# Kernel optimization log

Hardware: AMD Instinct MI355X
Metric: run time of the kernel (lower is better)

## Reference

```python
import jax, jax.numpy as jnp
import numpy as np

N_HEAD = 16
N_EMBD = 1024
HEAD_DIM = N_EMBD // N_HEAD
ROPE_BASE = 10000.0


def _rms_norm(x):
    # F.rms_norm with eps=None uses dtype eps
    eps = jnp.finfo(x.dtype).eps
    ms = jnp.mean(jnp.square(x), axis=-1, keepdims=True)
    return x * jax.lax.rsqrt(ms + eps)


def _rope_tables(T, dtype):
    inv_freq = 1.0 / (ROPE_BASE ** (jnp.arange(0, HEAD_DIM, 2, dtype=jnp.float32) / HEAD_DIM))
    t = jnp.arange(T, dtype=jnp.float32)
    freqs = jnp.outer(t, inv_freq)  # [T, D/2]
    cos = jnp.cos(freqs).astype(dtype)[None, :, None, :]  # [1,T,1,D/2]
    sin = jnp.sin(freqs).astype(dtype)[None, :, None, :]
    return cos, sin


def _apply_rotary(x, cos, sin):
    d = x.shape[-1] // 2
    x1, x2 = x[..., :d], x[..., d:]
    y1 = x1 * cos + x2 * sin
    y2 = -x1 * sin + x2 * cos
    return jnp.concatenate([y1, y2], axis=-1).astype(x.dtype)


def setup_inputs() -> dict:
    key = jax.random.key(0)
    ks = jax.random.split(key, 7)
    B, T, C = 4, 2048, N_EMBD
    s = 0.02
    return {
        "x": jax.random.normal(ks[0], (B, T, C), dtype=jnp.float32),
        "v1": jax.random.normal(ks[1], (B, T, C), dtype=jnp.float32),
        "Wq": jax.random.normal(ks[2], (C, C), dtype=jnp.float32) * s,
        "Wk": jax.random.normal(ks[3], (C, C), dtype=jnp.float32) * s,
        "Wv": jax.random.normal(ks[4], (C, C), dtype=jnp.float32) * s,
        "Wproj": jax.random.normal(ks[5], (C, C), dtype=jnp.float32) * s,
        "lamb": jnp.float32(0.5),
    }


def reference(x, v1, Wq, Wk, Wv, Wproj, lamb):
    B, T, C = x.shape
    H, D = N_HEAD, HEAD_DIM
    q = (x @ Wq.T).reshape(B, T, H, D)
    k = (x @ Wk.T).reshape(B, T, H, D)
    v = (x @ Wv.T).reshape(B, T, H, D)
    # value-lambda residual mix
    v = (1.0 - lamb) * v + lamb * v1.reshape(B, T, H, D)
    # RMSNorm then RoPE on q, k
    cos, sin = _rope_tables(T, x.dtype)
    q = _apply_rotary(_rms_norm(q), cos, sin)
    k = _apply_rotary(_rms_norm(k), cos, sin)
    # causal SDPA
    scale = 1.0 / jnp.sqrt(jnp.float32(D)).astype(x.dtype)
    scores = jnp.einsum("bthd,bshd->bhts", q, k) * scale  # [B,H,T,T]
    causal = jnp.tril(jnp.ones((T, T), dtype=bool))
    scores = jnp.where(causal[None, None], scores, jnp.finfo(scores.dtype).min)
    attn = jax.nn.softmax(scores, axis=-1)
    y = jnp.einsum("bhts,bshd->bthd", attn, v).reshape(B, T, C)
    y = y @ Wproj.T
    return (y, v1)
```

## Files before the change

kernel.cpp:

```cpp
#include <hip/hip_runtime.h>
#include <hip/hip_bf16.h>

typedef __bf16 bf16x8 __attribute__((ext_vector_type(8)));
typedef __bf16 bf16x4 __attribute__((ext_vector_type(4)));
typedef float  f32x4  __attribute__((ext_vector_type(4)));
typedef unsigned u32x4 __attribute__((ext_vector_type(4)));

#define B_ 4
#define T_ 2048
#define H_ 16
#define D_ 64
#define C_ 1024
#define M_ 8192
#define NE_ ((size_t)M_ * C_)

__global__ void probe_dtype(const unsigned short* __restrict__ x,
                            int* __restrict__ flag)
{
  __shared__ float red[256];
  float m = 0.0f;
  for (int i = threadIdx.x; i < 4096; i += 256) {
    unsigned int u = ((unsigned int)x[i]) << 16;
    float v = fabsf(__uint_as_float(u));
    if (!(v <= 1e30f)) v = 1e31f;
    m = fmaxf(m, v);
  }
  red[threadIdx.x] = m;
  __syncthreads();
  for (int s = 128; s > 0; s >>= 1) {
    if (threadIdx.x < s) red[threadIdx.x] = fmaxf(red[threadIdx.x], red[threadIdx.x + s]);
    __syncthreads();
  }
  if (threadIdx.x == 0) *flag = (red[0] > 100.0f) ? 1 : 0;
}

__device__ __forceinline__ float load1_adapt(const void* p, size_t idx, int f)
{
  if (f) return ((const float*)p)[idx];
  return __bfloat162float(((const __hip_bfloat16*)p)[idx]);
}

__global__ __launch_bounds__(256) void cvt_bf16(
    const int* __restrict__ flagp, const void* __restrict__ src,
    __bf16* __restrict__ dst, int n)
{
  const int f = *flagp;
  for (size_t i = ((size_t)blockIdx.x * 256 + threadIdx.x) * 8; i < (size_t)n;
       i += (size_t)gridDim.x * 2048) {
    bf16x8 r;
    if (f) {
      const float* pf = (const float*)src + i;
      float4 a = *(const float4*)pf;
      float4 b = *(const float4*)(pf + 4);
      r[0] = (__bf16)a.x; r[1] = (__bf16)a.y; r[2] = (__bf16)a.z; r[3] = (__bf16)a.w;
      r[4] = (__bf16)b.x; r[5] = (__bf16)b.y; r[6] = (__bf16)b.z; r[7] = (__bf16)b.w;
    } else {
      r = *(const bf16x8*)((const __bf16*)src + i);
    }
    *(bf16x8*)(dst + i) = r;
  }
}

__device__ __forceinline__ void g2lds16(const __bf16* g, __bf16* l)
{
  __builtin_amdgcn_global_load_lds(
      (const __attribute__((address_space(1))) void*)g,
      (__attribute__((address_space(3))) void*)l, 16, 0, 0);
}

__device__ __forceinline__ unsigned cvtpk_bf16(float lo, float hi)
{
  unsigned r;
  asm("v_cvt_pk_bf16_f32 %0, %1, %2" : "=v"(r) : "v"(lo), "v"(hi));
  return r;
}

__global__ __launch_bounds__(256) void gemm128(
    const __bf16* __restrict__ A, const __bf16* __restrict__ Bm,
    void* __restrict__ C, int M, int N, int K,
    const int* __restrict__ flagp, int adaptive)
{
  __shared__ __bf16 As[128][64];
  __shared__ __bf16 Bs[128][64];

  const int tid  = threadIdx.x;
  const int wv   = tid >> 6;
  const int lane = tid & 63;
  const int n16  = lane & 15;
  const int quad = lane >> 4;
  const int wm = (wv & 1) * 64, wn = (wv >> 1) * 64;

  const int nwgx = gridDim.x;
  const int id   = blockIdx.y * nwgx + blockIdx.x;
  const int cpx  = (nwgx * gridDim.y) >> 3;
  const int swz  = (id & 7) * cpx + (id >> 3);
  const int m0 = (swz % nwgx) * 128, n0 = (swz / nwgx) * 128;

  f32x4 acc[4][4];
#pragma unroll
  for (int i = 0; i < 4; i++)
#pragma unroll
    for (int j = 0; j < 4; j++) acc[i][j] = (f32x4){0.f, 0.f, 0.f, 0.f};

  const int trow = tid >> 3;
  const int tcol = (tid & 7) * 8;

  for (int k0 = 0; k0 < K; k0 += 64) {
#pragma unroll
    for (int p = 0; p < 4; p++) {
      g2lds16(A  + (size_t)(m0 + trow + p * 32) * K + k0 + tcol,
              &As[trow + p * 32][tcol]);
      g2lds16(Bm + (size_t)(n0 + trow + p * 32) * K + k0 + tcol,
              &Bs[trow + p * 32][tcol]);
    }
    __syncthreads();

#pragma unroll
    for (int kk = 0; kk < 2; kk++) {
      bf16x8 af[4], bf[4];
#pragma unroll
      for (int i = 0; i < 4; i++) {
        af[i] = *(const bf16x8*)&As[wm + i * 16 + n16][kk * 32 + quad * 8];
        bf[i] = *(const bf16x8*)&Bs[wn + i * 16 + n16][kk * 32 + quad * 8];
      }
#pragma unroll
      for (int i = 0; i < 4; i++)
#pragma unroll
        for (int j = 0; j < 4; j++)
          acc[i][j] = __builtin_amdgcn_mfma_f32_16x16x32_bf16(af[i], bf[j],
                                                              acc[i][j], 0, 0, 0);
    }
    __syncthreads();
  }

  const int f = adaptive ? *flagp : 0;
  const int rb = quad * 4;
#pragma unroll
  for (int i = 0; i < 4; i++)
#pragma unroll
    for (int j = 0; j < 4; j++)
#pragma unroll
      for (int r = 0; r < 4; r++) {
        const size_t idx = (size_t)(m0 + wm + i * 16 + rb + r) * N
                           + n0 + wn + j * 16 + n16;
        if (f) ((float*)C)[idx] = acc[i][j][r];
        else   ((__bf16*)C)[idx] = (__bf16)acc[i][j][r];
      }
}

__global__ __launch_bounds__(256) void fuse_rope_vmix(
    const int* __restrict__ flagp,
    __hip_bfloat16* __restrict__ q,
    __hip_bfloat16* __restrict__ k,
    __hip_bfloat16* __restrict__ v,
    const void* __restrict__ v1,
    const void* __restrict__ lambp)
{
  const int f    = *flagp;
  const int task = blockIdx.x * 4 + (threadIdx.x >> 6);
  const int lane = threadIdx.x & 63;
  const int h  = task & 15;
  const int bt = task >> 4;
  const int t  = bt & (T_ - 1);
  const size_t base = (size_t)bt * C_ + h * D_ + lane;

  const int j = lane & 31;
  const float inv = expf(-(float)j * (9.2103403719761836f / 32.0f));
  const float ang = (float)t * inv;
  const float cs = cosf(ang), sn = sinf(ang);
  const float EPS = 0.0078125f;

  {
    float xv = __bfloat162float(q[base]);
    float ss = xv * xv;
#pragma unroll
    for (int off = 32; off >= 1; off >>= 1) ss += __shfl_xor(ss, off);
    float r  = rsqrtf(ss * (1.0f / 64.0f) + EPS);
    float xn = xv * r;
    float pr = __shfl_xor(xn, 32);
    float yv = (lane < 32) ? (xn * cs + pr * sn) : (pr * -sn + xn * cs);
    q[base] = __float2bfloat16(yv);
  }
  {
    float xv = __bfloat162float(k[base]);
    float ss = xv * xv;
#pragma unroll
    for (int off = 32; off >= 1; off >>= 1) ss += __shfl_xor(ss, off);
    float r  = rsqrtf(ss * (1.0f / 64.0f) + EPS);
    float xn = xv * r;
    float pr = __shfl_xor(xn, 32);
    float yv = (lane < 32) ? (xn * cs + pr * sn) : (pr * -sn + xn * cs);
    k[base] = __float2bfloat16(yv);
  }
  {
    float lam = load1_adapt(lambp, 0, f);
    float vv  = __bfloat162float(v[base]);
    float v1v = load1_adapt(v1, base, f);
    v[base] = __float2bfloat16((1.0f - lam) * vv + lam * v1v);
  }
}

__global__ __launch_bounds__(256) void attn_mfma(
    const __bf16* q,
    const __bf16* __restrict__ k,
    const __bf16* __restrict__ v,
    __bf16* y)
{
  __shared__ alignas(16) __bf16 Ks[64][72];
  __shared__ alignas(16) __bf16 VTs[64][88];

  const int tid  = threadIdx.x;
  const int wv   = tid >> 6;
  const int lane = tid & 63;
  const int n16  = lane & 15;
  const int quad = lane >> 4;
  const int b = blockIdx.y >> 4, h = blockIdx.y & 15;
  const int q0 = (gridDim.x - 1 - blockIdx.x) * 128;
  const size_t hb = (size_t)b * T_ * C_ + h * D_;

  bf16x8 aq[2][2];
#pragma unroll
  for (int rt = 0; rt < 2; rt++) {
    const size_t qoff = hb + (size_t)(q0 + wv * 32 + rt * 16 + n16) * C_;
    aq[rt][0] = *(const bf16x8*)(q + qoff + quad * 8);
    aq[rt][1] = *(const bf16x8*)(q + qoff + 32 + quad * 8);
#pragma unroll
    for (int jj = 0; jj < 8; jj++) {
      aq[rt][0][jj] = (__bf16)((float)aq[rt][0][jj] * 0.125f);
      aq[rt][1][jj] = (__bf16)((float)aq[rt][1][jj] * 0.125f);
    }
  }

  f32x4 Ot[2][4];
  float l_lane[2];
#pragma unroll
  for (int rt = 0; rt < 2; rt++) {
    l_lane[rt] = 0.0f;
#pragma unroll
    for (int t = 0; t < 4; t++) Ot[rt][t] = (f32x4){0.f, 0.f, 0.f, 0.f};
  }

  const int trow = tid >> 2;
  const int tcol = (tid & 3) * 16;

  const int srcA = n16 + 32 * (quad & 1);
  const int srcB = srcA + 16;
  const bool lowq = quad < 2;

  const int niter = q0 / 64 + 2;

  bf16x8 kr0, kr1, vr0, vr1;
  {
    const __bf16* ks = k + hb + (size_t)trow * C_ + tcol;
    kr0 = *(const bf16x8*)(ks);
    kr1 = *(const bf16x8*)(ks + 8);
    const __bf16* vs = v + hb + (size_t)lane * C_;
    vr0 = *(const bf16x8*)(vs + wv * 8);
    vr1 = *(const bf16x8*)(vs + (wv + 4) * 8);
    *(bf16x8*)&Ks[trow][tcol]     = kr0;
    *(bf16x8*)&Ks[trow][tcol + 8] = kr1;
#pragma unroll
    for (int jj = 0; jj < 8; jj++) VTs[wv * 8 + jj][lane] = vr0[jj];
#pragma unroll
    for (int jj = 0; jj < 8; jj++) VTs[(wv + 4) * 8 + jj][lane] = vr1[jj];
  }
  __syncthreads();

  for (int it = 0; it < niter; it++) {
    const int s0 = it * 64;
    const bool havenext = (it + 1 < niter);

    if (havenext) {
      const int sn = s0 + 64;
      const __bf16* ks = k + hb + (size_t)(sn + trow) * C_ + tcol;
      kr0 = *(const bf16x8*)(ks);
      kr1 = *(const bf16x8*)(ks + 8);
      const __bf16* vs = v + hb + (size_t)(sn + lane) * C_;
      vr0 = *(const bf16x8*)(vs + wv * 8);
      vr1 = *(const bf16x8*)(vs + (wv + 4) * 8);
    }

    if (s0 <= q0 + wv * 32 + 31) {
#pragma unroll
      for (int rt = 0; rt < 2; rt++) {
        const int rbase = q0 + wv * 32 + rt * 16;
        if (s0 <= rbase + 15) {
          f32x4 S[4];
          __builtin_amdgcn_s_setprio(1);
#pragma unroll
          for (int t = 0; t < 4; t++) {
            S[t] = (f32x4){0.f, 0.f, 0.f, 0.f};
            bf16x8 b0 = *(const bf16x8*)&Ks[t * 16 + n16][quad * 8];
            bf16x8 b1 = *(const bf16x8*)&Ks[t * 16 + n16][32 + quad * 8];
            S[t] = __builtin_amdgcn_mfma_f32_16x16x32_bf16(b0, aq[rt][0], S[t], 0, 0, 0);
            S[t] = __builtin_amdgcn_mfma_f32_16x16x32_bf16(b1, aq[rt][1], S[t], 0, 0, 0);
          }
          __builtin_amdgcn_s_setprio(0);

          if (s0 + 63 > rbase) {
            const int tg = rbase + n16;
#pragma unroll
            for (int t = 0; t < 4; t++) {
#pragma unroll
              for (int r = 0; r < 4; r++) {
                const int sg = s0 + t * 16 + quad * 4 + r;
                if (sg > tg) S[t][r] = -1e30f;
              }
            }
          }

          float p[4][4];
#pragma unroll
          for (int t = 0; t < 4; t++)
#pragma unroll
            for (int r = 0; r < 4; r++)
              p[t][r] = __expf(S[t][r] - 8.0f);
          l_lane[rt] += ((p[0][0] + p[0][1]) + (p[0][2] + p[0][3]))
                      + ((p[1][0] + p[1][1]) + (p[1][2] + p[1][3]))
                      + ((p[2][0] + p[2][1]) + (p[2][2] + p[2][3]))
                      + ((p[3][0] + p[3][1]) + (p[3][2] + p[3][3]));

          unsigned pk0[4], pk1[4];
#pragma unroll
          for (int t = 0; t < 4; t++) {
            pk0[t] = cvtpk_bf16(p[t][0], p[t][1]);
            pk1[t] = cvtpk_bf16(p[t][2], p[t][3]);
          }

          bf16x8 pf[2];
#pragma unroll
          for (int c = 0; c < 2; c++) {
            const int tE = 2 * c, tO = 2 * c + 1;
            unsigned a0 = (unsigned)__shfl((int)pk0[tE], srcA);
            unsigned a1 = (unsigned)__shfl((int)pk0[tO], srcA);
            unsigned b0 = (unsigned)__shfl((int)pk1[tE], srcA);
            unsigned b1 = (unsigned)__shfl((int)pk1[tO], srcA);
            unsigned c0 = (unsigned)__shfl((int)pk0[tE], srcB);
            unsigned c1 = (unsigned)__shfl((int)pk0[tO], srcB);
            unsigned d0 = (unsigned)__shfl((int)pk1[tE], srcB);
            unsigned d1 = (unsigned)__shfl((int)pk1[tO], srcB);
            union { u32x4 u; bf16x8 b; } uw;
            uw.u[0] = lowq ? a0 : a1;
            uw.u[1] = lowq ? b0 : b1;
            uw.u[2] = lowq ? c0 : c1;
            uw.u[3] = lowq ? d0 : d1;
            pf[c] = uw.b;
          }

          __builtin_amdgcn_s_setprio(1);
#pragma unroll
          for (int t = 0; t < 4; t++) {
            bf16x8 va0 = *(const bf16x8*)&VTs[t * 16 + n16][quad * 8];
            bf16x8 va1 = *(const bf16x8*)&VTs[t * 16 + n16][32 + quad * 8];
            Ot[rt][t] = __builtin_amdgcn_mfma_f32_16x16x32_bf16(va0, pf[0], Ot[rt][t], 0, 0, 0);
            Ot[rt][t] = __builtin_amdgcn_mfma_f32_16x16x32_bf16(va1, pf[1], Ot[rt][t], 0, 0, 0);
          }
          __builtin_amdgcn_s_setprio(0);
        }
      }
    }

    __syncthreads();
    if (havenext) {
      *(bf16x8*)&Ks[trow][tcol]     = kr0;
      *(bf16x8*)&Ks[trow][tcol + 8] = kr1;
#pragma unroll
      for (int jj = 0; jj < 8; jj++) VTs[wv * 8 + jj][lane] = vr0[jj];
#pragma unroll
      for (int jj = 0; jj < 8; jj++) VTs[(wv + 4) * 8 + jj][lane] = vr1[jj];
    }
    __syncthreads();
  }

#pragma unroll
  for (int rt = 0; rt < 2; rt++) {
    float lt = l_lane[rt];
    lt += __shfl_xor(lt, 16);
    lt += __shfl_xor(lt, 32);
    const float linv = 1.0f / lt;
    const int qrow = q0 + wv * 32 + rt * 16 + n16;
#pragma unroll
    for (int t = 0; t < 4; t++) {
      bf16x4 o;
#pragma unroll
      for (int r = 0; r < 4; r++) o[r] = (__bf16)(Ot[rt][t][r] * linv);
      *(bf16x4*)(y + hb + (size_t)qrow * C_ + t * 16 + quad * 4) = o;
    }
  }
}

__global__ __launch_bounds__(256) void copy_v1(
    const int* __restrict__ flagp, const void* __restrict__ v1, void* __restrict__ out)
{
  const int f = *flagp;
  const size_t nbytes = NE_ * (f ? 4u : 2u);
  const uint4* s = (const uint4*)v1;
  uint4* d = (uint4*)((char*)out + nbytes);
  const size_t n16 = nbytes / 16;
  for (size_t i = (size_t)blockIdx.x * 256 + threadIdx.x; i < n16;
       i += (size_t)gridDim.x * 256)
    d[i] = s[i];
}

extern "C" void kernel_launch(void* const* d_in, const int* in_sizes, int n_in,
                              void* d_out, int out_size, void* d_ws, size_t ws_size,
                              hipStream_t stream)
{
  const void* x    = d_in[0];
  const void* v1   = d_in[1];
  const void* Wq   = d_in[2];
  const void* Wk   = d_in[3];
  const void* Wv   = d_in[4];
  const void* Wp   = d_in[5];
  const void* lamb = d_in[6];

  __bf16* xb  = (__bf16*)d_ws;
  __bf16* qw  = xb + NE_;
  __bf16* wqb = qw + NE_;
  __bf16* wkb = wqb + (size_t)C_ * C_;
  __bf16* wvb = wkb + (size_t)C_ * C_;
  __bf16* wpb = wvb + (size_t)C_ * C_;
  int* flagp  = (int*)(wpb + (size_t)C_ * C_);
  __bf16* kw = (__bf16*)d_out;
  __bf16* vw = (__bf16*)((char*)d_out + NE_ * 2);

  probe_dtype<<<1, 256, 0, stream>>>((const unsigned short*)x, flagp);

  cvt_bf16<<<4096, 256, 0, stream>>>(flagp, x,  xb,  (int)NE_);
  cvt_bf16<<<512,  256, 0, stream>>>(flagp, Wq, wqb, C_ * C_);
  cvt_bf16<<<512,  256, 0, stream>>>(flagp, Wk, wkb, C_ * C_);
  cvt_bf16<<<512,  256, 0, stream>>>(flagp, Wv, wvb, C_ * C_);
  cvt_bf16<<<512,  256, 0, stream>>>(flagp, Wp, wpb, C_ * C_);

  dim3 gg(M_ / 128, C_ / 128);
  gemm128<<<gg, 256, 0, stream>>>(xb, wqb, qw, M_, C_, C_, flagp, 0);
  gemm128<<<gg, 256, 0, stream>>>(xb, wkb, kw, M_, C_, C_, flagp, 0);
  gemm128<<<gg, 256, 0, stream>>>(xb, wvb, vw, M_, C_, C_, flagp, 0);

  fuse_rope_vmix<<<(M_ * H_) / 4, 256, 0, stream>>>(
      flagp, (__hip_bfloat16*)qw, (__hip_bfloat16*)kw, (__hip_bfloat16*)vw,
      v1, lamb);

  attn_mfma<<<dim3(T_ / 128, B_ * H_), 256, 0, stream>>>(qw, kw, vw, qw);

  gemm128<<<gg, 256, 0, stream>>>(qw, wpb, d_out, M_, C_, C_, flagp, 1);
  copy_v1<<<8192, 256, 0, stream>>>(flagp, v1, d_out);
}
```

Measured before the change: 454.6 us.

## Pre-transpose V and load K/V fragments directly from global in attention

Adds a separate kernel that transposes V into a per-head [D,T] layout in the now-free xb workspace. The attention kernel drops its shared-memory K/V staging and the two barriers per iteration, and instead loads MFMA operand fragments straight from global memory, relying on L2 reuse. Each wave now runs its own causal iteration count, and the block index is remapped so neighbouring blocks work on different heads. Launch bounds request 3 blocks per CU. The cost is an extra transpose pass over V, more global/L2 traffic per wave since waves no longer share staged tiles, and no software prefetch to hide load latency.

```diff
diff --git a/kernel.cpp b/kernel.cpp
--- a/kernel.cpp
+++ b/kernel.cpp
@@ -200,23 +200,50 @@
   }
 }
 
-__global__ __launch_bounds__(256) void attn_mfma(
+__global__ __launch_bounds__(256) void transp_v(
+    const __bf16* __restrict__ v, __bf16* __restrict__ vt)
+{
+  __shared__ __bf16 Ts[64][72];
+  const int bh = blockIdx.y;
+  const int t0 = blockIdx.x * 64;
+  const int b = bh >> 4, h = bh & 15;
+
+  const int r = threadIdx.x >> 2;
+  const int c = (threadIdx.x & 3) * 16;
+  const __bf16* src = v + (size_t)(b * T_ + t0 + r) * C_ + h * D_ + c;
+  *(bf16x8*)&Ts[r][c]     = *(const bf16x8*)src;
+  *(bf16x8*)&Ts[r][c + 8] = *(const bf16x8*)(src + 8);
+  __syncthreads();
+
+  const int d  = threadIdx.x >> 2;
+  const int tc = (threadIdx.x & 3) * 16;
+  bf16x8 o0, o1;
+#pragma unroll
+  for (int jj = 0; jj < 8; jj++) { o0[jj] = Ts[tc + jj][d]; o1[jj] = Ts[tc + 8 + jj][d]; }
+  __bf16* dst = vt + (size_t)(bh * D_ + d) * T_ + t0 + tc;
+  *(bf16x8*)dst       = o0;
+  *(bf16x8*)(dst + 8) = o1;
+}
+
+__global__ __launch_bounds__(256, 3) void attn_mfma(
     const __bf16* q,
     const __bf16* __restrict__ k,
-    const __bf16* __restrict__ v,
+    const __bf16* __restrict__ vt,
     __bf16* y)
 {
-  __shared__ alignas(16) __bf16 Ks[64][72];
-  __shared__ alignas(16) __bf16 VTs[64][88];
-
   const int tid  = threadIdx.x;
   const int wv   = tid >> 6;
   const int lane = tid & 63;
   const int n16  = lane & 15;
   const int quad = lane >> 4;
-  const int b = blockIdx.y >> 4, h = blockIdx.y & 15;
-  const int q0 = (gridDim.x - 1 - blockIdx.x) * 128;
-  const size_t hb = (size_t)b * T_ * C_ + h * D_;
+
+  const int id = blockIdx.y * gridDim.x + blockIdx.x;
+  const int bh = (id & 7) + 8 * ((id >> 3) & 7);
+  const int bx = id >> 6;
+  const int b = bh >> 4, h = bh & 15;
+  const int q0 = (gridDim.x - 1 - bx) * 128;
+  const size_t hb  = (size_t)b * T_ * C_ + h * D_;
+  const size_t vhb = (size_t)bh * D_ * T_;
 
   bf16x8 aq[2][2];
 #pragma unroll
@@ -240,136 +267,100 @@
     for (int t = 0; t < 4; t++) Ot[rt][t] = (f32x4){0.f, 0.f, 0.f, 0.f};
   }
 
-  const int trow = tid >> 2;
-  const int tcol = (tid & 3) * 16;
-
   const int srcA = n16 + 32 * (quad & 1);
   const int srcB = srcA + 16;
   const bool lowq = quad < 2;
 
-  const int niter = q0 / 64 + 2;
-
-  bf16x8 kr0, kr1, vr0, vr1;
-  {
-    const __bf16* ks = k + hb + (size_t)trow * C_ + tcol;
-    kr0 = *(const bf16x8*)(ks);
-    kr1 = *(const bf16x8*)(ks + 8);
-    const __bf16* vs = v + hb + (size_t)lane * C_;
-    vr0 = *(const bf16x8*)(vs + wv * 8);
-    vr1 = *(const bf16x8*)(vs + (wv + 4) * 8);
-    *(bf16x8*)&Ks[trow][tcol]     = kr0;
-    *(bf16x8*)&Ks[trow][tcol + 8] = kr1;
-#pragma unroll
-    for (int jj = 0; jj < 8; jj++) VTs[wv * 8 + jj][lane] = vr0[jj];
-#pragma unroll
-    for (int jj = 0; jj < 8; jj++) VTs[(wv + 4) * 8 + jj][lane] = vr1[jj];
-  }
-  __syncthreads();
+  const int rbase0 = q0 + wv * 32;
+  const int niter  = (rbase0 + 31) / 64 + 1;
 
   for (int it = 0; it < niter; it++) {
     const int s0 = it * 64;
-    const bool havenext = (it + 1 < niter);
-
-    if (havenext) {
-      const int sn = s0 + 64;
-      const __bf16* ks = k + hb + (size_t)(sn + trow) * C_ + tcol;
-      kr0 = *(const bf16x8*)(ks);
-      kr1 = *(const bf16x8*)(ks + 8);
-      const __bf16* vs = v + hb + (size_t)(sn + lane) * C_;
-      vr0 = *(const bf16x8*)(vs + wv * 8);
-      vr1 = *(const bf16x8*)(vs + (wv + 4) * 8);
-    }
-
-    if (s0 <= q0 + wv * 32 + 31) {
-#pragma unroll
-      for (int rt = 0; rt < 2; rt++) {
-        const int rbase = q0 + wv * 32 + rt * 16;
-        if (s0 <= rbase + 15) {
-          f32x4 S[4];
-          __builtin_amdgcn_s_setprio(1);
+
+    bf16x8 kf[4][2], vf[4][2];
+#pragma unroll
+    for (int t = 0; t < 4; t++) {
+      const __bf16* kp = k + hb + (size_t)(s0 + t * 16 + n16) * C_;
+      kf[t][0] = *(const bf16x8*)(kp + quad * 8);
+      kf[t][1] = *(const bf16x8*)(kp + 32 + quad * 8);
+      const __bf16* vp = vt + vhb + (size_t)(t * 16 + n16) * T_ + s0;
+      vf[t][0] = *(const bf16x8*)(vp + quad * 8);
+      vf[t][1] = *(const bf16x8*)(vp + 32 + quad * 8);
+    }
+
+#pragma unroll
+    for (int rt = 0; rt < 2; rt++) {
+      const int rbase = rbase0 + rt * 16;
+      if (s0 <= rbase + 15) {
+        f32x4 S[4];
+        __builtin_amdgcn_s_setprio(1);
+#pragma unroll
+        for (int t = 0; t < 4; t++) {
+          S[t] = (f32x4){0.f, 0.f, 0.f, 0.f};
+          S[t] = __builtin_amdgcn_mfma_f32_16x16x32_bf16(kf[t][0], aq[rt][0], S[t], 0, 0, 0);
+          S[t] = __builtin_amdgcn_mfma_f32_16x16x32_bf16(kf[t][1], aq[rt][1], S[t], 0, 0, 0);
+        }
+        __builtin_amdgcn_s_setprio(0);
+
+        if (s0 + 63 > rbase) {
+          const int tg = rbase + n16;
 #pragma unroll
           for (int t = 0; t < 4; t++) {
-            S[t] = (f32x4){0.f, 0.f, 0.f, 0.f};
-            bf16x8 b0 = *(const bf16x8*)&Ks[t * 16 + n16][quad * 8];
-            bf16x8 b1 = *(const bf16x8*)&Ks[t * 16 + n16][32 + quad * 8];
-            S[t] = __builtin_amdgcn_mfma_f32_16x16x32_bf16(b0, aq[rt][0], S[t], 0, 0, 0);
-            S[t] = __builtin_amdgcn_mfma_f32_16x16x32_bf16(b1, aq[rt][1], S[t], 0, 0, 0);
-          }
-          __builtin_amdgcn_s_setprio(0);
-
-          if (s0 + 63 > rbase) {
-            const int tg = rbase + n16;
-#pragma unroll
-            for (int t = 0; t < 4; t++) {
-#pragma unroll
-              for (int r = 0; r < 4; r++) {
-                const int sg = s0 + t * 16 + quad * 4 + r;
-                if (sg > tg) S[t][r] = -1e30f;
-              }
+#pragma unroll
+            for (int r = 0; r < 4; r++) {
+              const int sg = s0 + t * 16 + quad * 4 + r;
+              if (sg > tg) S[t][r] = -1e30f;
             }
           }
-
-          float p[4][4];
-#pragma unroll
-          for (int t = 0; t < 4; t++)
-#pragma unroll
-            for (int r = 0; r < 4; r++)
-              p[t][r] = __expf(S[t][r] - 8.0f);
-          l_lane[rt] += ((p[0][0] + p[0][1]) + (p[0][2] + p[0][3]))
-                      + ((p[1][0] + p[1][1]) + (p[1][2] + p[1][3]))
-                      + ((p[2][0] + p[2][1]) + (p[2][2] + p[2][3]))
-                      + ((p[3][0] + p[3][1]) + (p[3][2] + p[3][3]));
-
-          unsigned pk0[4], pk1[4];
-#pragma unroll
-          for (int t = 0; t < 4; t++) {
-            pk0[t] = cvtpk_bf16(p[t][0], p[t][1]);
-            pk1[t] = cvtpk_bf16(p[t][2], p[t][3]);
-          }
-
-          bf16x8 pf[2];
-#pragma unroll
-          for (int c = 0; c < 2; c++) {
-            const int tE = 2 * c, tO = 2 * c + 1;
-            unsigned a0 = (unsigned)__shfl((int)pk0[tE], srcA);
-            unsigned a1 = (unsigned)__shfl((int)pk0[tO], srcA);
-            unsigned b0 = (unsigned)__shfl((int)pk1[tE], srcA);
-            unsigned b1 = (unsigned)__shfl((int)pk1[tO], srcA);
-            unsigned c0 = (unsigned)__shfl((int)pk0[tE], srcB);
-            unsigned c1 = (unsigned)__shfl((int)pk0[tO], srcB);
-            unsigned d0 = (unsigned)__shfl((int)pk1[tE], srcB);
-            unsigned d1 = (unsigned)__shfl((int)pk1[tO], srcB);
-            union { u32x4 u; bf16x8 b; } uw;
-            uw.u[0] = lowq ? a0 : a1;
-            uw.u[1] = lowq ? b0 : b1;
-            uw.u[2] = lowq ? c0 : c1;
-            uw.u[3] = lowq ? d0 : d1;
-            pf[c] = uw.b;
-          }
-
-          __builtin_amdgcn_s_setprio(1);
-#pragma unroll
-          for (int t = 0; t < 4; t++) {
-            bf16x8 va0 = *(const bf16x8*)&VTs[t * 16 + n16][quad * 8];
-            bf16x8 va1 = *(const bf16x8*)&VTs[t * 16 + n16][32 + quad * 8];
-            Ot[rt][t] = __builtin_amdgcn_mfma_f32_16x16x32_bf16(va0, pf[0], Ot[rt][t], 0, 0, 0);
-            Ot[rt][t] = __builtin_amdgcn_mfma_f32_16x16x32_bf16(va1, pf[1], Ot[rt][t], 0, 0, 0);
-          }
-          __builtin_amdgcn_s_setprio(0);
         }
+
+        float p[4][4];
+#pragma unroll
+        for (int t = 0; t < 4; t++)
+#pragma unroll
+          for (int r = 0; r < 4; r++)
+            p[t][r] = __expf(S[t][r] - 8.0f);
+        l_lane[rt] += ((p[0][0] + p[0][1]) + (p[0][2] + p[0][3]))
+                    + ((p[1][0] + p[1][1]) + (p[1][2] + p[1][3]))
+                    + ((p[2][0] + p[2][1]) + (p[2][2] + p[2][3]))
+                    + ((p[3][0] + p[3][1]) + (p[3][2] + p[3][3]));
+
+        unsigned pk0[4], pk1[4];
+#pragma unroll
+        for (int t = 0; t < 4; t++) {
+          pk0[t] = cvtpk_bf16(p[t][0], p[t][1]);
+          pk1[t] = cvtpk_bf16(p[t][2], p[t][3]);
+        }
+
+        bf16x8 pf[2];
+#pragma unroll
+        for (int c = 0; c < 2; c++) {
+          const int tE = 2 * c, tO = 2 * c + 1;
+          unsigned a0 = (unsigned)__shfl((int)pk0[tE], srcA);
+          unsigned a1 = (unsigned)__shfl((int)pk0[tO], srcA);
+          unsigned b0 = (unsigned)__shfl((int)pk1[tE], srcA);
+          unsigned b1 = (unsigned)__shfl((int)pk1[tO], srcA);
+          unsigned c0 = (unsigned)__shfl((int)pk0[tE], srcB);
+          unsigned c1 = (unsigned)__shfl((int)pk0[tO], srcB);
+          unsigned d0 = (unsigned)__shfl((int)pk1[tE], srcB);
+          unsigned d1 = (unsigned)__shfl((int)pk1[tO], srcB);
+          union { u32x4 u; bf16x8 bv; } uw;
+          uw.u[0] = lowq ? a0 : a1;
+          uw.u[1] = lowq ? b0 : b1;
+          uw.u[2] = lowq ? c0 : c1;
+          uw.u[3] = lowq ? d0 : d1;
+          pf[c] = uw.bv;
+        }
+
+        __builtin_amdgcn_s_setprio(1);
+#pragma unroll
+        for (int t = 0; t < 4; t++) {
+          Ot[rt][t] = __builtin_amdgcn_mfma_f32_16x16x32_bf16(vf[t][0], pf[0], Ot[rt][t], 0, 0, 0);
+          Ot[rt][t] = __builtin_amdgcn_mfma_f32_16x16x32_bf16(vf[t][1], pf[1], Ot[rt][t], 0, 0, 0);
+        }
+        __builtin_amdgcn_s_setprio(0);
       }
     }
-
-    __syncthreads();
-    if (havenext) {
-      *(bf16x8*)&Ks[trow][tcol]     = kr0;
-      *(bf16x8*)&Ks[trow][tcol + 8] = kr1;
-#pragma unroll
-      for (int jj = 0; jj < 8; jj++) VTs[wv * 8 + jj][lane] = vr0[jj];
-#pragma unroll
-      for (int jj = 0; jj < 8; jj++) VTs[(wv + 4) * 8 + jj][lane] = vr1[jj];
-    }
-    __syncthreads();
   }
 
 #pragma unroll
@@ -421,6 +412,7 @@
   __bf16* wvb = wkb + (size_t)C_ * C_;
   __bf16* wpb = wvb + (size_t)C_ * C_;
   int* flagp  = (int*)(wpb + (size_t)C_ * C_);
+  __bf16* vtb = xb;
   __bf16* kw = (__bf16*)d_out;
   __bf16* vw = (__bf16*)((char*)d_out + NE_ * 2);
 
@@ -441,7 +433,9 @@
       flagp, (__hip_bfloat16*)qw, (__hip_bfloat16*)kw, (__hip_bfloat16*)vw,
       v1, lamb);
 
-  attn_mfma<<<dim3(T_ / 128, B_ * H_), 256, 0, stream>>>(qw, kw, vw, qw);
+  transp_v<<<dim3(T_ / 64, B_ * H_), 256, 0, stream>>>(vw, vtb);
+
+  attn_mfma<<<dim3(T_ / 128, B_ * H_), 256, 0, stream>>>(qw, kw, vtb, qw);
 
   gemm128<<<gg, 256, 0, stream>>>(qw, wpb, d_out, M_, C_, C_, flagp, 1);
   copy_v1<<<8192, 256, 0, stream>>>(flagp, v1, d_out);
```

Measured after the change: 448.7 us. About the same (-1.3%).
